# Kernel optimization log

Measured on AMD Instinct MI355X. Metric: run time of the kernel, lower is better.

Reference implementation:

```python
import jax, jax.numpy as jnp
import numpy as np

B, F, D = 32768, 2668, 64

def _xn(key, shape):
    # xavier_normal_: std = sqrt(2/(fan_in+fan_out))
    std = np.sqrt(2.0 / (shape[0] + shape[1]))
    return jax.random.normal(key, shape, dtype=jnp.float32) * std

def setup_inputs() -> dict:
    key = jax.random.key(0)
    ks = jax.random.split(key, 16)
    fv = jax.random.uniform(ks[0], (B, F), dtype=jnp.float32)
    sizes = [(1, 'age_user_w'), (1, 'age_item_w'), (2, 'gender_user_w'), (2, 'gender_item_w'),
             (21, 'occupation_user_w'), (21, 'occupation_item_w'), (19, 'movie_user_w'), (19, 'movie_item_w'),
             (943, 'userid_user_w'), (943, 'userid_item_w'), (1682, 'itemid_user_w'), (1682, 'itemid_item_w')]
    inp = {'feature_vector': fv}
    for i, (n, name) in enumerate(sizes):
        inp[name] = _xn(ks[i + 1], (n, D))
    # nn.Linear(F,1): kaiming-uniform weight, uniform bias; plain uniform scale suffices for a reference
    bound = 1.0 / np.sqrt(F)
    inp['lin_w'] = jax.random.uniform(ks[13], (1, F), dtype=jnp.float32, minval=-bound, maxval=bound)
    inp['lin_b'] = jax.random.uniform(ks[14], (1,), dtype=jnp.float32, minval=-bound, maxval=bound)
    return inp

def reference(feature_vector, age_user_w, age_item_w, gender_user_w, gender_item_w,
              occupation_user_w, occupation_item_w, movie_user_w, movie_item_w,
              userid_user_w, userid_item_w, itemid_user_w, itemid_item_w, lin_w, lin_b):
    fv = feature_vector
    au = fv[:, 2626:2627] @ age_user_w          # [B, D] (note: column 2626 reused, as in source)
    ai = fv[:, 2626:2627] @ age_item_w
    gu = fv[:, 2626:2628] @ gender_user_w
    gi = fv[:, 2626:2628] @ gender_item_w
    ou = fv[:, 2628:2649] @ occupation_user_w
    oi = fv[:, 2628:2649] @ occupation_item_w
    mu = fv[:, 2649:2668] @ movie_user_w
    mi = fv[:, 2649:2668] @ movie_item_w
    uu = fv[:, 0:943] @ userid_user_w
    ui = fv[:, 0:943] @ userid_item_w
    tu = fv[:, 943:2625] @ itemid_user_w
    ti = fv[:, 943:2625] @ itemid_item_w
    cross = jnp.sum(au * gu + au * ou + ai * mu + au * uu + ai * tu
                    + gu * ou + gi * mu + gu * uu + gi * tu
                    + oi * mu + ou * uu + oi * tu
                    + mu * ui + mi * ti + ui * tu, axis=1)   # [B]
    logits = fv @ lin_w.T + lin_b + cross[:, None]           # [B, 1]
    return jax.nn.sigmoid(logits)
```

## Files before the change

kernel.cpp:

```cpp
#include <hip/hip_runtime.h>

#define FDIM 2668

typedef float f32x4 __attribute__((ext_vector_type(4)));
typedef _Float16 f16x8 __attribute__((ext_vector_type(8)));

#define G1_NK 30
#define G2_NK 53
#define G3_NK 2
#define G1_NT 9
#define G2_NT 9
#define G3_NT 29
#define BUF_BYTES (G3_NT * 1024)

#define HU 0
#define HT (G1_NK * G1_NT * 512)
#define HS (HT + G2_NK * G2_NT * 512)
#define H_TOTAL (HS + G3_NK * G3_NT * 512)

__global__ __launch_bounds__(256) void ffm_prep(
    const float* __restrict__ au_, const float* __restrict__ ai_,
    const float* __restrict__ gu_, const float* __restrict__ gi_,
    const float* __restrict__ ou_, const float* __restrict__ oi_,
    const float* __restrict__ mu_, const float* __restrict__ mi_,
    const float* __restrict__ uu_, const float* __restrict__ ui_,
    const float* __restrict__ tu_, const float* __restrict__ ti_,
    const float* __restrict__ lw, _Float16* __restrict__ ws) {
  int e = blockIdx.x * 256 + threadIdx.x;
  if (e >= H_TOTAL) return;
  float val = 0.f;
  int rel, ntiles;
  if (e < HT) { rel = e; ntiles = G1_NT; }
  else if (e < HS) { rel = e - HT; ntiles = G2_NT; }
  else { rel = e - HS; ntiles = G3_NT; }
  int perk = ntiles * 512;
  int kb = rel / perk;
  int r = rel - kb * perk;
  int nt = r >> 9; r &= 511;
  int lane = r >> 3, j = r & 7;
  int k = kb * 32 + ((lane >> 4) << 3) + j;
  int n = (nt << 4) + (lane & 15);

  if (e < HT) {
    if (k < 943) {
      if (n < 64) val = uu_[k * 64 + n];
      else if (n < 128) val = ui_[k * 64 + n - 64];
      else if (n == 128) val = lw[k];
    }
  } else if (e < HS) {
    int col = 940 + k;
    if (n < 64) { if (col >= 943 && col < 2625) val = tu_[(col - 943) * 64 + n]; }
    else if (n < 128) { if (col >= 943 && col < 2625) val = ti_[(col - 943) * 64 + n - 64]; }
    else if (n == 128) { if (col >= 943 && col <= 2635) val = lw[col]; }
  } else {
    int col = 2624 + k;
    if (n == 448) { if (col >= 2636 && col < 2668) val = lw[col]; }
    else if (n < 448) {
      int blk = n >> 6, d = n & 63;
      float ageu = (col == 2626) ? au_[d] : 0.f;
      float agei = (col == 2626) ? ai_[d] : 0.f;
      float genu = (col >= 2626 && col < 2628) ? gu_[(col - 2626) * 64 + d] : 0.f;
      float geni = (col >= 2626 && col < 2628) ? gi_[(col - 2626) * 64 + d] : 0.f;
      float occu = (col >= 2628 && col < 2649) ? ou_[(col - 2628) * 64 + d] : 0.f;
      float occi = (col >= 2628 && col < 2649) ? oi_[(col - 2628) * 64 + d] : 0.f;
      float movu = (col >= 2649 && col < 2668) ? mu_[(col - 2649) * 64 + d] : 0.f;
      float movi = (col >= 2649 && col < 2668) ? mi_[(col - 2649) * 64 + d] : 0.f;
      switch (blk) {
        case 0: val = ageu + genu + occu; break;
        case 1: val = agei + geni + occi; break;
        case 2: val = movu; break;
        case 3: val = movi; break;
        case 4: val = ageu; break;
        case 5: val = genu; break;
        case 6: val = occu; break;
      }
    }
  }
  ws[e] = (_Float16)val;
}

template <int NT>
__device__ __forceinline__ void stageB(const _Float16* __restrict__ src, char* lds,
                                       int bufOff, int tid, int wave) {
  constexpr int chunks = NT * 64;
#pragma unroll
  for (int base = 0; base < chunks; base += 256) {
    int idx = base + tid;
    if (idx < chunks) {
      __builtin_amdgcn_global_load_lds(
          (const __attribute__((address_space(1))) void*)(src + (size_t)idx * 8),
          (__attribute__((address_space(3))) void*)(lds + bufOff + (base + wave * 64) * 16),
          16, 0, 0);
    }
  }
}

template <bool GUARD>
__device__ __forceinline__ void loadA(f32x4& a0, f32x4& a1,
                                      const float* __restrict__ myrow, int c0) {
  f32x4 z = {0.f, 0.f, 0.f, 0.f};
  if (!GUARD || (c0 + 4) <= FDIM) a0 = *(const f32x4*)(myrow + c0); else a0 = z;
  if (!GUARD || (c0 + 8) <= FDIM) a1 = *(const f32x4*)(myrow + c0 + 4); else a1 = z;
}

template <int NT, bool GUARD>
__device__ __forceinline__ void gemm_phase(const float* __restrict__ myrow, int colbase,
                                           int nk, const _Float16* __restrict__ wsrc,
                                           char* lds, int tid, int lane, int kg, int wave,
                                           f32x4* acc) {
  stageB<NT>(wsrc, lds, 0, tid, wave);
  f32x4 a0, a1;
  loadA<GUARD>(a0, a1, myrow, colbase + kg * 8);
  int cur = 0;
  for (int kb = 0; kb < nk; ++kb) {
    __syncthreads();
    f32x4 n0 = {0.f, 0.f, 0.f, 0.f}, n1 = {0.f, 0.f, 0.f, 0.f};
    if (kb + 1 < nk) {
      stageB<NT>(wsrc + (size_t)(kb + 1) * (NT * 512), lds, (cur ^ 1) * BUF_BYTES, tid, wave);
      loadA<GUARD>(n0, n1, myrow, colbase + (kb + 1) * 32 + kg * 8);
    }
    f16x8 af;
#pragma unroll
    for (int i = 0; i < 4; ++i) { af[i] = (_Float16)a0[i]; af[4 + i] = (_Float16)a1[i]; }
    const char* buf = lds + cur * BUF_BYTES + lane * 16;
#pragma unroll
    for (int nt = 0; nt < NT; ++nt) {
      f16x8 bf = *(const f16x8*)(buf + nt * 1024);
      acc[nt] = __builtin_amdgcn_mfma_f32_16x16x32_f16(af, bf, acc[nt], 0, 0, 0);
    }
    a0 = n0; a1 = n1;
    cur ^= 1;
  }
}

__global__ __launch_bounds__(256, 2) void ffm_main(
    const float* __restrict__ fv, const _Float16* __restrict__ wp,
    const float* __restrict__ linb, float* __restrict__ out) {
  __shared__ __align__(16) char lds[2 * BUF_BYTES];
  const int tid = threadIdx.x;
  const int lane = tid & 63;
  const int wave = tid >> 6;
  const int nl = lane & 15;
  const int kg = lane >> 4;
  const int rowbase = blockIdx.x * 64 + wave * 16;
  const float* myrow = fv + (size_t)(rowbase + nl) * FDIM;
  const f32x4 zero4 = {0.f, 0.f, 0.f, 0.f};

  f32x4 s[G3_NT];
#pragma unroll
  for (int i = 0; i < G3_NT; ++i) s[i] = zero4;
  gemm_phase<G3_NT, true>(myrow, 2624, G3_NK, wp + HS, lds, tid, lane, kg, wave, s);

  f32x4 P[4], Q[4], MU[4], MI[4];
  f32x4 cross = s[28];
#pragma unroll
  for (int t = 0; t < 4; ++t) {
    P[t] = s[t]; Q[t] = s[4 + t]; MU[t] = s[8 + t]; MI[t] = s[12 + t];
    cross += s[16 + t] * (s[20 + t] + s[24 + t]) + s[20 + t] * s[24 + t] + MU[t] * Q[t];
  }

  f32x4 u[G1_NT];
#pragma unroll
  for (int i = 0; i < G1_NT; ++i) u[i] = zero4;
  gemm_phase<G1_NT, false>(myrow, 0, G1_NK, wp + HU, lds, tid, lane, kg, wave, u);
  cross += u[8];
#pragma unroll
  for (int t = 0; t < 4; ++t) {
    cross += u[t] * P[t] + u[4 + t] * MU[t];
    Q[t] += u[4 + t];
  }

  f32x4 v[G2_NT];
#pragma unroll
  for (int i = 0; i < G2_NT; ++i) v[i] = zero4;
  gemm_phase<G2_NT, false>(myrow, 940, G2_NK, wp + HT, lds, tid, lane, kg, wave, v);
  cross += v[8];
#pragma unroll
  for (int t = 0; t < 4; ++t) {
    cross += v[t] * Q[t] + v[4 + t] * MI[t];
  }

  float c0 = cross[0], c1 = cross[1], c2 = cross[2], c3 = cross[3];
#pragma unroll
  for (int m = 1; m <= 8; m <<= 1) {
    c0 += __shfl_xor(c0, m, 64);
    c1 += __shfl_xor(c1, m, 64);
    c2 += __shfl_xor(c2, m, 64);
    c3 += __shfl_xor(c3, m, 64);
  }
  if (nl == 0) {
    float lb = linb[0];
    int r = rowbase + kg * 4;
    out[r + 0] = 1.f / (1.f + __expf(-(c0 + lb)));
    out[r + 1] = 1.f / (1.f + __expf(-(c1 + lb)));
    out[r + 2] = 1.f / (1.f + __expf(-(c2 + lb)));
    out[r + 3] = 1.f / (1.f + __expf(-(c3 + lb)));
  }
}

extern "C" void kernel_launch(void* const* d_in, const int* in_sizes, int n_in,
                              void* d_out, int out_size, void* d_ws, size_t ws_size,
                              hipStream_t stream) {
  const float* fv    = (const float*)d_in[0];
  const float* age_u = (const float*)d_in[1];
  const float* age_i = (const float*)d_in[2];
  const float* gen_u = (const float*)d_in[3];
  const float* gen_i = (const float*)d_in[4];
  const float* occ_u = (const float*)d_in[5];
  const float* occ_i = (const float*)d_in[6];
  const float* mov_u = (const float*)d_in[7];
  const float* mov_i = (const float*)d_in[8];
  const float* uid_u = (const float*)d_in[9];
  const float* uid_i = (const float*)d_in[10];
  const float* iid_u = (const float*)d_in[11];
  const float* iid_i = (const float*)d_in[12];
  const float* lin_w = (const float*)d_in[13];
  const float* lin_b = (const float*)d_in[14];
  _Float16* ws = (_Float16*)d_ws;
  float* out = (float*)d_out;

  ffm_prep<<<(H_TOTAL + 255) / 256, 256, 0, stream>>>(
      age_u, age_i, gen_u, gen_i, occ_u, occ_i, mov_u, mov_i,
      uid_u, uid_i, iid_u, iid_i, lin_w, ws);
  ffm_main<<<32768 / 64, 256, 0, stream>>>(fv, ws, lin_b, out);
}
```

Measured before the change: 504.7 us.

## Deepen GEMM pipeline to 4-stage LDS ring with 64-wide K super-steps

Replaces the double-buffered 32-wide K loop with a 4-slot LDS ring over 64-wide K super-steps. B tiles are prefetched three steps ahead with global_load_lds, A rows are prefetched two steps ahead, and hand-written vmcnt waits replace __syncthreads. The small tail phase is now staged in one shot with a single barrier. This is meant to hide global latency and halve barrier count, but it raises LDS use to about 72KB per block, which may limit occupancy. The vmcnt counts are fragile and depend on how many loads each wave issues.

```diff
diff --git a/kernel.cpp b/kernel.cpp
--- a/kernel.cpp
+++ b/kernel.cpp
@@ -6,17 +6,21 @@
 typedef _Float16 f16x8 __attribute__((ext_vector_type(8)));
 
 #define G1_NK 30
-#define G2_NK 53
+#define G2_NK 54
 #define G3_NK 2
 #define G1_NT 9
 #define G2_NT 9
 #define G3_NT 29
-#define BUF_BYTES (G3_NT * 1024)
+#define G1_NS 15
+#define G2_NS 27
 
 #define HU 0
 #define HT (G1_NK * G1_NT * 512)
 #define HS (HT + G2_NK * G2_NT * 512)
 #define H_TOTAL (HS + G3_NK * G3_NT * 512)
+
+#define SUPB (G1_NT * 2048)
+#define LDSB (4 * SUPB)
 
 __global__ __launch_bounds__(256) void ffm_prep(
     const float* __restrict__ au_, const float* __restrict__ ai_,
@@ -79,69 +83,107 @@
   ws[e] = (_Float16)val;
 }
 
+__device__ __forceinline__ void gll16(const _Float16* __restrict__ src, char* dst) {
+  __builtin_amdgcn_global_load_lds((const __attribute__((address_space(1))) void*)src,
+                                   (__attribute__((address_space(3))) void*)dst, 16, 0, 0);
+}
+
 template <int NT>
-__device__ __forceinline__ void stageB(const _Float16* __restrict__ src, char* lds,
+__device__ __forceinline__ void stageS(const _Float16* __restrict__ src, char* lds,
                                        int bufOff, int tid, int wave) {
-  constexpr int chunks = NT * 64;
+  constexpr int chunks = NT * 128;
 #pragma unroll
   for (int base = 0; base < chunks; base += 256) {
     int idx = base + tid;
-    if (idx < chunks) {
-      __builtin_amdgcn_global_load_lds(
-          (const __attribute__((address_space(1))) void*)(src + (size_t)idx * 8),
-          (__attribute__((address_space(3))) void*)(lds + bufOff + (base + wave * 64) * 16),
-          16, 0, 0);
-    }
-  }
+    if (idx < chunks)
+      gll16(src + (size_t)idx * 8, lds + bufOff + (base + wave * 64) * 16);
+  }
+}
+
+__device__ __forceinline__ void loadS(f32x4 (&A)[4], const float* __restrict__ myrow, int cs) {
+  A[0] = *(const f32x4*)(myrow + cs);
+  A[1] = *(const f32x4*)(myrow + cs + 4);
+  A[2] = *(const f32x4*)(myrow + cs + 32);
+  A[3] = *(const f32x4*)(myrow + cs + 36);
 }
 
 template <bool GUARD>
-__device__ __forceinline__ void loadA(f32x4& a0, f32x4& a1,
-                                      const float* __restrict__ myrow, int c0) {
+__device__ __forceinline__ f32x4 ldg4(const float* __restrict__ myrow, int c) {
   f32x4 z = {0.f, 0.f, 0.f, 0.f};
-  if (!GUARD || (c0 + 4) <= FDIM) a0 = *(const f32x4*)(myrow + c0); else a0 = z;
-  if (!GUARD || (c0 + 8) <= FDIM) a1 = *(const f32x4*)(myrow + c0 + 4); else a1 = z;
-}
-
-template <int NT, bool GUARD>
-__device__ __forceinline__ void gemm_phase(const float* __restrict__ myrow, int colbase,
-                                           int nk, const _Float16* __restrict__ wsrc,
-                                           char* lds, int tid, int lane, int kg, int wave,
-                                           f32x4* acc) {
-  stageB<NT>(wsrc, lds, 0, tid, wave);
-  f32x4 a0, a1;
-  loadA<GUARD>(a0, a1, myrow, colbase + kg * 8);
-  int cur = 0;
-  for (int kb = 0; kb < nk; ++kb) {
-    __syncthreads();
-    f32x4 n0 = {0.f, 0.f, 0.f, 0.f}, n1 = {0.f, 0.f, 0.f, 0.f};
-    if (kb + 1 < nk) {
-      stageB<NT>(wsrc + (size_t)(kb + 1) * (NT * 512), lds, (cur ^ 1) * BUF_BYTES, tid, wave);
-      loadA<GUARD>(n0, n1, myrow, colbase + (kb + 1) * 32 + kg * 8);
-    }
-    f16x8 af;
-#pragma unroll
-    for (int i = 0; i < 4; ++i) { af[i] = (_Float16)a0[i]; af[4 + i] = (_Float16)a1[i]; }
-    const char* buf = lds + cur * BUF_BYTES + lane * 16;
-#pragma unroll
-    for (int nt = 0; nt < NT; ++nt) {
-      f16x8 bf = *(const f16x8*)(buf + nt * 1024);
-      acc[nt] = __builtin_amdgcn_mfma_f32_16x16x32_f16(af, bf, acc[nt], 0, 0, 0);
-    }
-    a0 = n0; a1 = n1;
-    cur ^= 1;
+  if (!GUARD || (c + 4) <= FDIM) return *(const f32x4*)(myrow + c);
+  return z;
+}
+
+__device__ __forceinline__ void syncw(int sel, bool hiw) {
+  if (sel == 2) {
+    if (hiw) asm volatile("s_waitcnt vmcnt(14) lgkmcnt(0)" ::: "memory");
+    else     asm volatile("s_waitcnt vmcnt(12) lgkmcnt(0)" ::: "memory");
+  } else if (sel == 1) {
+    if (hiw) asm volatile("s_waitcnt vmcnt(9) lgkmcnt(0)" ::: "memory");
+    else     asm volatile("s_waitcnt vmcnt(8) lgkmcnt(0)" ::: "memory");
+  } else {
+    asm volatile("s_waitcnt vmcnt(0) lgkmcnt(0)" ::: "memory");
+  }
+  __builtin_amdgcn_s_barrier();
+}
+
+template <int NT, int NS>
+__device__ __forceinline__ void pbody(int k, f32x4 (&Au)[4], f32x4 (&An)[4],
+                                      const float* __restrict__ myrow, int colbase,
+                                      const _Float16* __restrict__ wsrc, char* lds,
+                                      int tid, int lane, int kg, int wave, bool hiw,
+                                      f32x4* acc) {
+  int sel = (k + 2 < NS) ? 2 : ((k + 1 < NS) ? 1 : 0);
+  syncw(sel, hiw);
+  if (k + 2 < NS) loadS(An, myrow, colbase + (k + 2) * 64 + kg * 8);
+  if (k + 3 < NS)
+    stageS<NT>(wsrc + (size_t)(k + 3) * (NT * 1024), lds, ((k + 3) & 3) * SUPB, tid, wave);
+  f16x8 af0, af1;
+#pragma unroll
+  for (int i = 0; i < 4; ++i) {
+    af0[i] = (_Float16)Au[0][i]; af0[4 + i] = (_Float16)Au[1][i];
+    af1[i] = (_Float16)Au[2][i]; af1[4 + i] = (_Float16)Au[3][i];
+  }
+  const char* buf = lds + ((k & 3) * SUPB) + lane * 16;
+#pragma unroll
+  for (int nt = 0; nt < NT; ++nt)
+    acc[nt] = __builtin_amdgcn_mfma_f32_16x16x32_f16(
+        af0, *(const f16x8*)(buf + nt * 1024), acc[nt], 0, 0, 0);
+#pragma unroll
+  for (int nt = 0; nt < NT; ++nt)
+    acc[nt] = __builtin_amdgcn_mfma_f32_16x16x32_f16(
+        af1, *(const f16x8*)(buf + NT * 1024 + nt * 1024), acc[nt], 0, 0, 0);
+}
+
+template <int NT, int NS>
+__device__ __forceinline__ void phaseP(const float* __restrict__ myrow, int colbase,
+                                       const _Float16* __restrict__ wsrc, char* lds,
+                                       int tid, int lane, int kg, int wave, bool hiw,
+                                       f32x4* acc) {
+  static_assert(NS % 3 == 0, "NS must be divisible by 3 for static A rotation");
+  f32x4 A0[4], A1[4], A2[4];
+  stageS<NT>(wsrc, lds, 0, tid, wave);
+  loadS(A0, myrow, colbase + kg * 8);
+  stageS<NT>(wsrc + (size_t)(NT * 1024), lds, SUPB, tid, wave);
+  loadS(A1, myrow, colbase + 64 + kg * 8);
+  stageS<NT>(wsrc + (size_t)2 * (NT * 1024), lds, 2 * SUPB, tid, wave);
+  for (int kb = 0; kb < NS; kb += 3) {
+    pbody<NT, NS>(kb + 0, A0, A2, myrow, colbase, wsrc, lds, tid, lane, kg, wave, hiw, acc);
+    pbody<NT, NS>(kb + 1, A1, A0, myrow, colbase, wsrc, lds, tid, lane, kg, wave, hiw, acc);
+    pbody<NT, NS>(kb + 2, A2, A1, myrow, colbase, wsrc, lds, tid, lane, kg, wave, hiw, acc);
   }
 }
 
 __global__ __launch_bounds__(256, 2) void ffm_main(
     const float* __restrict__ fv, const _Float16* __restrict__ wp,
     const float* __restrict__ linb, float* __restrict__ out) {
-  __shared__ __align__(16) char lds[2 * BUF_BYTES];
+  __shared__ __align__(16) char lds[LDSB];
   const int tid = threadIdx.x;
   const int lane = tid & 63;
   const int wave = tid >> 6;
   const int nl = lane & 15;
   const int kg = lane >> 4;
+  const bool hiw = tid < 128;
   const int rowbase = blockIdx.x * 64 + wave * 16;
   const float* myrow = fv + (size_t)(rowbase + nl) * FDIM;
   const f32x4 zero4 = {0.f, 0.f, 0.f, 0.f};
@@ -149,7 +191,38 @@
   f32x4 s[G3_NT];
 #pragma unroll
   for (int i = 0; i < G3_NT; ++i) s[i] = zero4;
-  gemm_phase<G3_NT, true>(myrow, 2624, G3_NK, wp + HS, lds, tid, lane, kg, wave, s);
+  {
+    constexpr int chunks = G3_NT * 64 * G3_NK;
+#pragma unroll
+    for (int base = 0; base < chunks; base += 256) {
+      int idx = base + tid;
+      if (idx < chunks)
+        gll16(wp + HS + (size_t)idx * 8, lds + (base + wave * 64) * 16);
+    }
+    f32x4 a0 = ldg4<true>(myrow, 2624 + kg * 8);
+    f32x4 a1 = ldg4<true>(myrow, 2624 + kg * 8 + 4);
+    f32x4 a2 = ldg4<true>(myrow, 2656 + kg * 8);
+    f32x4 a3 = ldg4<true>(myrow, 2656 + kg * 8 + 4);
+    asm volatile("s_waitcnt vmcnt(0) lgkmcnt(0)" ::: "memory");
+    __builtin_amdgcn_s_barrier();
+    f16x8 af0, af1;
+#pragma unroll
+    for (int i = 0; i < 4; ++i) {
+      af0[i] = (_Float16)a0[i]; af0[4 + i] = (_Float16)a1[i];
+      af1[i] = (_Float16)a2[i]; af1[4 + i] = (_Float16)a3[i];
+    }
+    const char* buf = lds + lane * 16;
+#pragma unroll
+    for (int nt = 0; nt < G3_NT; ++nt)
+      s[nt] = __builtin_amdgcn_mfma_f32_16x16x32_f16(
+          af0, *(const f16x8*)(buf + nt * 1024), s[nt], 0, 0, 0);
+#pragma unroll
+    for (int nt = 0; nt < G3_NT; ++nt)
+      s[nt] = __builtin_amdgcn_mfma_f32_16x16x32_f16(
+          af1, *(const f16x8*)(buf + G3_NT * 1024 + nt * 1024), s[nt], 0, 0, 0);
+    asm volatile("s_waitcnt lgkmcnt(0)" ::: "memory");
+    __builtin_amdgcn_s_barrier();
+  }
 
   f32x4 P[4], Q[4], MU[4], MI[4];
   f32x4 cross = s[28];
@@ -162,23 +235,24 @@
   f32x4 u[G1_NT];
 #pragma unroll
   for (int i = 0; i < G1_NT; ++i) u[i] = zero4;
-  gemm_phase<G1_NT, false>(myrow, 0, G1_NK, wp + HU, lds, tid, lane, kg, wave, u);
+  phaseP<G1_NT, G1_NS>(myrow, 0, wp + HU, lds, tid, lane, kg, wave, hiw, u);
   cross += u[8];
 #pragma unroll
   for (int t = 0; t < 4; ++t) {
     cross += u[t] * P[t] + u[4 + t] * MU[t];
     Q[t] += u[4 + t];
   }
+  asm volatile("s_waitcnt lgkmcnt(0)" ::: "memory");
+  __builtin_amdgcn_s_barrier();
 
   f32x4 v[G2_NT];
 #pragma unroll
   for (int i = 0; i < G2_NT; ++i) v[i] = zero4;
-  gemm_phase<G2_NT, false>(myrow, 940, G2_NK, wp + HT, lds, tid, lane, kg, wave, v);
+  phaseP<G2_NT, G2_NS>(myrow, 940, wp + HT, lds, tid, lane, kg, wave, hiw, v);
   cross += v[8];
 #pragma unroll
-  for (int t = 0; t < 4; ++t) {
+  for (int t = 0; t < 4; ++t)
     cross += v[t] * Q[t] + v[4 + t] * MI[t];
-  }
 
   float c0 = cross[0], c1 = cross[1], c2 = cross[2], c3 = cross[3];
 #pragma unroll
```

Measured after the change: 505.6 us. No clear change (+0.2%).
